# Optimization experiments

Measured on AMD Instinct MI355X. Metric: run time of the kernel, lower is better.

The kernel has to match this reference:

```python
import jax, jax.numpy as jnp
import numpy as np

EMB = 1024
HID = 1024
VOCAB = 32000
SEQ = 128


def _lstm_cell(x, h, c, W_ih, W_hh, b_ih, b_hh):
    # PyTorch gate order: input, forget, cell(g), output
    gates = x @ W_ih.T + b_ih + h @ W_hh.T + b_hh  # [4H]
    i, f, g, o = jnp.split(gates, 4)
    c_new = jax.nn.sigmoid(f) * c + jax.nn.sigmoid(i) * jnp.tanh(g)
    h_new = jax.nn.sigmoid(o) * jnp.tanh(c_new)
    return h_new, c_new


def setup_inputs() -> dict:
    key = jax.random.key(0)
    ks = jax.random.split(key, 12)
    s_emb = 0.02
    s_lstm = 1.0 / np.sqrt(HID)
    return {
        "sentence": jax.random.randint(ks[0], (SEQ,), 0, VOCAB),
        "given_num": 64,
        "emb": jax.random.normal(ks[1], (VOCAB, EMB), jnp.float32) * s_emb,
        "W_ih_lstm": jax.random.normal(ks[2], (4 * HID, EMB), jnp.float32) * s_lstm,
        "W_hh_lstm": jax.random.normal(ks[3], (4 * HID, HID), jnp.float32) * s_lstm,
        "b_ih_lstm": jax.random.normal(ks[4], (4 * HID,), jnp.float32) * s_lstm,
        "b_hh_lstm": jax.random.normal(ks[5], (4 * HID,), jnp.float32) * s_lstm,
        "W_ih_cell": jax.random.normal(ks[6], (4 * HID, EMB), jnp.float32) * s_lstm,
        "W_hh_cell": jax.random.normal(ks[7], (4 * HID, HID), jnp.float32) * s_lstm,
        "b_ih_cell": jax.random.normal(ks[8], (4 * HID,), jnp.float32) * s_lstm,
        "b_hh_cell": jax.random.normal(ks[9], (4 * HID,), jnp.float32) * s_lstm,
        "W_tag": jax.random.normal(ks[10], (VOCAB, HID), jnp.float32) * s_lstm,
        "b_tag": jax.random.normal(ks[11], (VOCAB,), jnp.float32) * s_lstm,
    }


def reference(sentence, given_num, emb, W_ih_lstm, W_hh_lstm, b_ih_lstm, b_hh_lstm,
              W_ih_cell, W_hh_cell, b_ih_cell, b_hh_cell, W_tag, b_tag):
    given_num = int(given_num)  # static (batch-1 rollout, fixed split point)

    # ---- teacher-forced prefix through nn.LSTM (init_hidden -> zeros) ----
    embeds_existing = emb[sentence[:given_num]]  # [g, E]

    def prefix_step(carry, x):
        h, c = carry
        h, c = _lstm_cell(x, h, c, W_ih_lstm, W_hh_lstm, b_ih_lstm, b_hh_lstm)
        return (h, c), h

    h0 = jnp.zeros((HID,), embeds_existing.dtype)
    (h, c), lstm_out = jax.lax.scan(prefix_step, (h0, h0), embeds_existing)
    tag_prefix = lstm_out @ W_tag.T + b_tag  # [g, V]

    # multinomial over softmax(tag) == categorical over logits; only last row's
    # sample is consumed as x_t
    skeys = jax.random.split(jax.random.key(123), SEQ - given_num + 1)
    x_t = jax.random.categorical(skeys[0], tag_prefix[-1])

    def rollout_step(carry, k):
        x_t, h, c = carry
        e = emb[x_t]
        h, c = _lstm_cell(e, h, c, W_ih_cell, W_hh_cell, b_ih_cell, b_hh_cell)
        logits = h @ W_tag.T + b_tag  # [V]
        x_next = jax.random.categorical(k, logits)
        return (x_next, h, c), logits

    _, tag_roll = jax.lax.scan(rollout_step, (x_t, h, c), skeys[1:])  # [S-g, V]

    tag_space = jnp.concatenate([tag_prefix, tag_roll], axis=0)  # [S, V]
    return jax.nn.log_softmax(tag_space, axis=-1)
```

## Files before the change

kernel.cpp:

```cpp
#include <hip/hip_runtime.h>
#include <cstdint>
#include <cstddef>

#define EMBD 1024
#define HIDD 1024
#define G4   4096
#define VOC  32000
#define SEQL 128
#define GN   64
#define NR   64

#define JAX_PARTITIONABLE 1

__device__ __forceinline__ uint32_t rotl32(uint32_t v, int d) { return (v << d) | (v >> (32 - d)); }

__device__ inline void threefry2x32(uint32_t k0, uint32_t k1, uint32_t x0, uint32_t x1,
                                    uint32_t& o0, uint32_t& o1) {
  uint32_t ks2 = k0 ^ k1 ^ 0x1BD11BDAu;
#define TF_ROUND(r) { x0 += x1; x1 = rotl32(x1, r); x1 ^= x0; }
  x0 += k0;  x1 += k1;
  TF_ROUND(13) TF_ROUND(15) TF_ROUND(26) TF_ROUND(6)
  x0 += k1;  x1 += ks2 + 1u;
  TF_ROUND(17) TF_ROUND(29) TF_ROUND(16) TF_ROUND(24)
  x0 += ks2; x1 += k0 + 2u;
  TF_ROUND(13) TF_ROUND(15) TF_ROUND(26) TF_ROUND(6)
  x0 += k0;  x1 += k1 + 3u;
  TF_ROUND(17) TF_ROUND(29) TF_ROUND(16) TF_ROUND(24)
  x0 += k1;  x1 += ks2 + 4u;
  TF_ROUND(13) TF_ROUND(15) TF_ROUND(26) TF_ROUND(6)
  x0 += ks2; x1 += k0 + 5u;
#undef TF_ROUND
  o0 = x0; o1 = x1;
}

__device__ inline uint32_t rng_bits(uint32_t k0, uint32_t k1, uint32_t idx) {
#if JAX_PARTITIONABLE
  uint32_t h0, h1; threefry2x32(k0, k1, 0u, idx, h0, h1);
  return h0 ^ h1;
#else
  uint32_t h0, h1;
  if (idx < (VOC / 2)) { threefry2x32(k0, k1, idx, idx + (VOC / 2), h0, h1); return h0; }
  else                 { threefry2x32(k0, k1, idx - (VOC / 2), idx, h0, h1); return h1; }
#endif
}

__device__ inline float gumbel_of(uint32_t k0, uint32_t k1, uint32_t idx) {
  uint32_t bits = rng_bits(k0, k1, idx);
  float u = __uint_as_float((bits >> 9) | 0x3f800000u) - 1.0f;
  u = fmaxf(u, 1.17549435e-38f);
  return -logf(-logf(u));
}

__device__ inline unsigned long long packCand(float v, int idx) {
  uint32_t u = __float_as_uint(v);
  u = (u & 0x80000000u) ? ~u : (u | 0x80000000u);
  return ((unsigned long long)u << 32) | (unsigned long long)(0xFFFFFFFFu - (uint32_t)idx);
}

__device__ inline float sigf(float x) { return 1.0f / (1.0f + expf(-x)); }

__global__ void k_init(uint2* keys, unsigned* counters, float* cbuf, float* h0) {
  int t = threadIdx.x;
#if JAX_PARTITIONABLE
  if (t < NR + 1) {
    uint32_t a, b; threefry2x32(0u, 123u, 0u, (uint32_t)t, a, b);
    keys[t] = make_uint2(a, b);
  }
#else
  __shared__ uint32_t buf[2 * (NR + 1)];
  if (t < NR + 1) {
    uint32_t a, b; threefry2x32(0u, 123u, (uint32_t)t, (uint32_t)(t + NR + 1), a, b);
    buf[t] = a; buf[t + NR + 1] = b;
  }
  __syncthreads();
  if (t < NR + 1) keys[t] = make_uint2(buf[2 * t], buf[2 * t + 1]);
#endif
  for (int i = t; i < 66; i += 256) counters[i] = 0u;
  for (int i = t; i < HIDD; i += 256) { cbuf[i] = 0.0f; h0[i] = 0.0f; }
}

__global__ void k_gather(const float* __restrict__ emb, const int* __restrict__ sent,
                         float* __restrict__ X) {
  int m = blockIdx.x;
  int row = sent[m];
  const float4* s = (const float4*)(emb + (size_t)row * EMBD);
  float4* d = (float4*)(X + (size_t)m * EMBD);
  d[threadIdx.x] = s[threadIdx.x];
}

__global__ __launch_bounds__(256) void k_gemm64(const float* __restrict__ A,
                                                const float* __restrict__ B,
                                                const float* __restrict__ bias,
                                                float* __restrict__ C, int ldc) {
  __shared__ float As[64][33];
  __shared__ float Bs[64][33];
  int n0 = blockIdx.x * 64;
  int tn = threadIdx.x & 15, tm = threadIdx.x >> 4;
  float acc[4][4] = {{0.f}};
  for (int k0 = 0; k0 < 1024; k0 += 32) {
    for (int f = threadIdx.x; f < 512; f += 256) {
      int r = f >> 3, c4 = (f & 7) << 2;
      float4 v = *(const float4*)(A + (size_t)r * 1024 + k0 + c4);
      As[r][c4 + 0] = v.x; As[r][c4 + 1] = v.y; As[r][c4 + 2] = v.z; As[r][c4 + 3] = v.w;
      float4 u = *(const float4*)(B + (size_t)(n0 + r) * 1024 + k0 + c4);
      Bs[r][c4 + 0] = u.x; Bs[r][c4 + 1] = u.y; Bs[r][c4 + 2] = u.z; Bs[r][c4 + 3] = u.w;
    }
    __syncthreads();
#pragma unroll
    for (int kk = 0; kk < 32; ++kk) {
      float a0 = As[tm * 4 + 0][kk], a1 = As[tm * 4 + 1][kk];
      float a2 = As[tm * 4 + 2][kk], a3 = As[tm * 4 + 3][kk];
      float b0 = Bs[tn * 4 + 0][kk], b1 = Bs[tn * 4 + 1][kk];
      float b2 = Bs[tn * 4 + 2][kk], b3 = Bs[tn * 4 + 3][kk];
      acc[0][0] += a0 * b0; acc[0][1] += a0 * b1; acc[0][2] += a0 * b2; acc[0][3] += a0 * b3;
      acc[1][0] += a1 * b0; acc[1][1] += a1 * b1; acc[1][2] += a1 * b2; acc[1][3] += a1 * b3;
      acc[2][0] += a2 * b0; acc[2][1] += a2 * b1; acc[2][2] += a2 * b2; acc[2][3] += a2 * b3;
      acc[3][0] += a3 * b0; acc[3][1] += a3 * b1; acc[3][2] += a3 * b2; acc[3][3] += a3 * b3;
    }
    __syncthreads();
  }
#pragma unroll
  for (int i = 0; i < 4; ++i)
#pragma unroll
    for (int j = 0; j < 4; ++j) {
      int m = tm * 4 + i, n = n0 + tn * 4 + j;
      float r = acc[i][j] + (bias ? bias[n] : 0.0f);
      C[(size_t)m * ldc + n] = r;
    }
}

__global__ __launch_bounds__(256) void k_lstm_pre(const float* __restrict__ Whh,
                                                  const float* __restrict__ bih,
                                                  const float* __restrict__ bhh,
                                                  const float* __restrict__ gx, int t,
                                                  const float* __restrict__ hprev,
                                                  float* __restrict__ cbuf,
                                                  float* __restrict__ hout) {
  __shared__ float gs[4];
  int wave = threadIdx.x >> 6, lane = threadIdx.x & 63;
  int j = blockIdx.x;
  int r = j + (wave << 10);
  const float4* h4 = (const float4*)hprev;
  const float4* w4 = (const float4*)(Whh + (size_t)r * 1024);
  float a = 0.0f;
#pragma unroll
  for (int q = 0; q < 4; ++q) {
    float4 w = w4[lane + (q << 6)];
    float4 h = h4[lane + (q << 6)];
    a += w.x * h.x + w.y * h.y + w.z * h.z + w.w * h.w;
  }
#pragma unroll
  for (int off = 32; off; off >>= 1) a += __shfl_xor(a, off, 64);
  if (lane == 0) gs[wave] = a + gx[(size_t)t * G4 + r] + bih[r] + bhh[r];
  __syncthreads();
  if (threadIdx.x == 0) {
    float gi = gs[0], gf = gs[1], gg = gs[2], go = gs[3];
    float cn = sigf(gf) * cbuf[j] + sigf(gi) * tanhf(gg);
    cbuf[j] = cn;
    hout[j] = sigf(go) * tanhf(cn);
  }
}

__global__ __launch_bounds__(256) void k_lstm_roll(const float* __restrict__ Wih,
                                                   const float* __restrict__ Whh,
                                                   const float* __restrict__ bih,
                                                   const float* __restrict__ bhh,
                                                   const float* __restrict__ emb,
                                                   const int* __restrict__ tok, int t,
                                                   const float* __restrict__ hprev,
                                                   float* __restrict__ cbuf,
                                                   float* __restrict__ hout) {
  __shared__ float gs[4];
  int wave = threadIdx.x >> 6, lane = threadIdx.x & 63;
  int j = blockIdx.x;
  int r = j + (wave << 10);
  int row = tok[t];
  const float4* x4 = (const float4*)(emb + (size_t)row * EMBD);
  const float4* h4 = (const float4*)hprev;
  const float4* wi = (const float4*)(Wih + (size_t)r * 1024);
  const float4* wh = (const float4*)(Whh + (size_t)r * 1024);
  float a = 0.0f;
#pragma unroll
  for (int q = 0; q < 4; ++q) {
    float4 w = wi[lane + (q << 6)];
    float4 x = x4[lane + (q << 6)];
    a += w.x * x.x + w.y * x.y + w.z * x.z + w.w * x.w;
    w = wh[lane + (q << 6)];
    float4 h = h4[lane + (q << 6)];
    a += w.x * h.x + w.y * h.y + w.z * h.z + w.w * h.w;
  }
#pragma unroll
  for (int off = 32; off; off >>= 1) a += __shfl_xor(a, off, 64);
  if (lane == 0) gs[wave] = a + bih[r] + bhh[r];
  __syncthreads();
  if (threadIdx.x == 0) {
    float gi = gs[0], gf = gs[1], gg = gs[2], go = gs[3];
    float cn = sigf(gf) * cbuf[j] + sigf(gi) * tanhf(gg);
    cbuf[j] = cn;
    hout[j] = sigf(go) * tanhf(cn);
  }
}

__global__ __launch_bounds__(256) void k_logits(const float* __restrict__ Wtag,
                                                const float* __restrict__ btag,
                                                const float* __restrict__ h,
                                                float* __restrict__ outrow,
                                                const uint2* __restrict__ keys, int key_idx,
                                                unsigned long long* __restrict__ partials,
                                                unsigned* __restrict__ counter,
                                                int* __restrict__ token_out) {
  __shared__ float sums[64];
  __shared__ unsigned long long red[256];
  __shared__ int amLast;
  int wave = threadIdx.x >> 6, lane = threadIdx.x & 63;
  int r0 = blockIdx.x * 64;
  const float4* h4 = (const float4*)h;
  float4 hv[4];
#pragma unroll
  for (int q = 0; q < 4; ++q) hv[q] = h4[lane + (q << 6)];
  for (int rr = 0; rr < 16; ++rr) {
    int lr = wave * 16 + rr;
    int r = r0 + lr;
    const float4* w4 = (const float4*)(Wtag + (size_t)r * 1024);
    float a = 0.0f;
#pragma unroll
    for (int q = 0; q < 4; ++q) {
      float4 w = w4[lane + (q << 6)];
      a += w.x * hv[q].x + w.y * hv[q].y + w.z * hv[q].z + w.w * hv[q].w;
    }
#pragma unroll
    for (int off = 32; off; off >>= 1) a += __shfl_xor(a, off, 64);
    if (lane == 0) sums[lr] = a;
  }
  __syncthreads();
  unsigned long long best = 0ull;
  if (threadIdx.x < 64) {
    int r = r0 + threadIdx.x;
    float L = sums[threadIdx.x] + btag[r];
    outrow[r] = L;
    uint2 K = keys[key_idx];
    float y = L + gumbel_of(K.x, K.y, (uint32_t)r);
    best = packCand(y, r);
#pragma unroll
    for (int off = 32; off; off >>= 1) {
      unsigned long long o = __shfl_xor(best, off, 64);
      if (o > best) best = o;
    }
    if (threadIdx.x == 0) partials[blockIdx.x] = best;
  }
  __threadfence();
  __syncthreads();
  if (threadIdx.x == 0) amLast = (atomicAdd(counter, 1u) == gridDim.x - 1) ? 1 : 0;
  __syncthreads();
  if (amLast) {
    __threadfence();
    unsigned long long b = 0ull;
    for (int i = threadIdx.x; i < (int)gridDim.x; i += 256) {
      unsigned long long v = *((volatile unsigned long long*)(partials + i));
      if (v > b) b = v;
    }
    red[threadIdx.x] = b;
    __syncthreads();
    for (int s = 128; s; s >>= 1) {
      if (threadIdx.x < s) {
        if (red[threadIdx.x + s] > red[threadIdx.x]) red[threadIdx.x] = red[threadIdx.x + s];
      }
      __syncthreads();
    }
    if (threadIdx.x == 0)
      token_out[0] = (int)(0xFFFFFFFFu - (uint32_t)(red[0] & 0xFFFFFFFFull));
  }
}

__global__ __launch_bounds__(256) void k_sample_row(const float* __restrict__ row,
                                                    const uint2* __restrict__ keys, int key_idx,
                                                    unsigned long long* __restrict__ partials,
                                                    unsigned* __restrict__ counter,
                                                    int* __restrict__ token_out) {
  __shared__ unsigned long long red[256];
  __shared__ int amLast;
  int v = blockIdx.x * 256 + threadIdx.x;
  unsigned long long best = 0ull;
  if (v < VOC) {
    uint2 K = keys[key_idx];
    float y = row[v] + gumbel_of(K.x, K.y, (uint32_t)v);
    best = packCand(y, v);
  }
  red[threadIdx.x] = best;
  __syncthreads();
  for (int s = 128; s; s >>= 1) {
    if (threadIdx.x < s) {
      if (red[threadIdx.x + s] > red[threadIdx.x]) red[threadIdx.x] = red[threadIdx.x + s];
    }
    __syncthreads();
  }
  if (threadIdx.x == 0) partials[blockIdx.x] = red[0];
  __threadfence();
  __syncthreads();
  if (threadIdx.x == 0) amLast = (atomicAdd(counter, 1u) == gridDim.x - 1) ? 1 : 0;
  __syncthreads();
  if (amLast) {
    __threadfence();
    unsigned long long b = 0ull;
    for (int i = threadIdx.x; i < (int)gridDim.x; i += 256) {
      unsigned long long val = *((volatile unsigned long long*)(partials + i));
      if (val > b) b = val;
    }
    red[threadIdx.x] = b;
    __syncthreads();
    for (int s = 128; s; s >>= 1) {
      if (threadIdx.x < s) {
        if (red[threadIdx.x + s] > red[threadIdx.x]) red[threadIdx.x] = red[threadIdx.x + s];
      }
      __syncthreads();
    }
    if (threadIdx.x == 0)
      token_out[0] = (int)(0xFFFFFFFFu - (uint32_t)(red[0] & 0xFFFFFFFFull));
  }
}

__global__ __launch_bounds__(256) void k_logsoftmax(float* __restrict__ C) {
  __shared__ float red[256];
  float* row = C + (size_t)blockIdx.x * VOC;
  float m = -INFINITY;
  for (int i = threadIdx.x; i < VOC; i += 256) m = fmaxf(m, row[i]);
  red[threadIdx.x] = m;
  __syncthreads();
  for (int s = 128; s; s >>= 1) {
    if (threadIdx.x < s) red[threadIdx.x] = fmaxf(red[threadIdx.x], red[threadIdx.x + s]);
    __syncthreads();
  }
  m = red[0];
  __syncthreads();
  float sum = 0.0f;
  for (int i = threadIdx.x; i < VOC; i += 256) sum += expf(row[i] - m);
  red[threadIdx.x] = sum;
  __syncthreads();
  for (int s = 128; s; s >>= 1) {
    if (threadIdx.x < s) red[threadIdx.x] += red[threadIdx.x + s];
    __syncthreads();
  }
  float lse = m + logf(red[0]);
  __syncthreads();
  for (int i = threadIdx.x; i < VOC; i += 256) row[i] = row[i] - lse;
}

extern "C" void kernel_launch(void* const* d_in, const int* in_sizes, int n_in,
                              void* d_out, int out_size, void* d_ws, size_t ws_size,
                              hipStream_t stream) {
  (void)in_sizes; (void)n_in; (void)out_size; (void)ws_size;
  const int*   sent  = (const int*)  d_in[0];
  const float* emb   = (const float*)d_in[2];
  const float* Wih_l = (const float*)d_in[3];
  const float* Whh_l = (const float*)d_in[4];
  const float* bih_l = (const float*)d_in[5];
  const float* bhh_l = (const float*)d_in[6];
  const float* Wih_c = (const float*)d_in[7];
  const float* Whh_c = (const float*)d_in[8];
  const float* bih_c = (const float*)d_in[9];
  const float* bhh_c = (const float*)d_in[10];
  const float* Wtag  = (const float*)d_in[11];
  const float* btag  = (const float*)d_in[12];
  float* out = (float*)d_out;

  char* ws = (char*)d_ws;
  uint2*              keys     = (uint2*)(ws + 0);
  int*                tokens   = (int*)(ws + 1024);
  unsigned*           counters = (unsigned*)(ws + 2048);
  unsigned long long* partials = (unsigned long long*)(ws + 4096);
  float*              cbuf     = (float*)(ws + 8192);
  float*              h0       = (float*)(ws + 12288);
  float*              lstm_out = (float*)(ws + 16384);
  float*              hroll    = (float*)(ws + 16384 + 262144);
  float*              X        = (float*)(ws + 16384 + 2 * 262144);
  float*              gx       = (float*)(ws + 16384 + 3 * 262144);

  k_init<<<1, 256, 0, stream>>>(keys, counters, cbuf, h0);
  k_gather<<<GN, 256, 0, stream>>>(emb, sent, X);
  k_gemm64<<<G4 / 64, 256, 0, stream>>>(X, Wih_l, nullptr, gx, G4);
  for (int t = 0; t < GN; ++t) {
    const float* hp = t ? (lstm_out + (size_t)(t - 1) * HIDD) : h0;
    k_lstm_pre<<<HIDD, 256, 0, stream>>>(Whh_l, bih_l, bhh_l, gx, t, hp, cbuf,
                                         lstm_out + (size_t)t * HIDD);
  }
  k_gemm64<<<VOC / 64, 256, 0, stream>>>(lstm_out, Wtag, btag, out, VOC);
  k_sample_row<<<(VOC + 255) / 256, 256, 0, stream>>>(out + (size_t)(GN - 1) * VOC, keys, 0,
                                                      partials, counters + 64, tokens);
  for (int t = 0; t < NR; ++t) {
    const float* hp = t ? (hroll + (size_t)(t - 1) * HIDD) : (lstm_out + (size_t)(GN - 1) * HIDD);
    k_lstm_roll<<<HIDD, 256, 0, stream>>>(Wih_c, Whh_c, bih_c, bhh_c, emb, tokens, t, hp, cbuf,
                                          hroll + (size_t)t * HIDD);
    k_logits<<<VOC / 64, 256, 0, stream>>>(Wtag, btag, hroll + (size_t)t * HIDD,
                                           out + (size_t)(GN + t) * VOC, keys, 1 + t,
                                           partials, counters + t, tokens + t + 1);
  }
  k_logsoftmax<<<SEQL, 256, 0, stream>>>(out);
}
```

Before: 5.351 ms.

## Store W_tag as fp16 for logits GEMV and prefix GEMM

Each call converts the vocabulary projection matrix W_tag once to fp16 in workspace. The prefix GEMM and the per-step rollout logits kernel then read the half-size copy and accumulate in fp32. The rollout kernel is rewritten as a wave-per-row GEMV over 32 rows per block, with the partials area enlarged to fit more blocks. The goal is to halve the memory traffic of the bandwidth-bound per-token logits pass. The cost is an extra conversion pass, and the rounded weights may flip sampled tokens relative to the fp32 reference.

```diff
diff --git a/kernel.cpp b/kernel.cpp
--- a/kernel.cpp
+++ b/kernel.cpp
@@ -1,4 +1,5 @@
 #include <hip/hip_runtime.h>
+#include <hip/hip_fp16.h>
 #include <cstdint>
 #include <cstddef>
 
@@ -59,6 +60,11 @@
 
 __device__ inline float sigf(float x) { return 1.0f / (1.0f + expf(-x)); }
 
+__device__ __forceinline__ float h2f(unsigned short u) {
+  __half_raw hr; hr.x = u;
+  return __half2float(__half(hr));
+}
+
 __global__ void k_init(uint2* keys, unsigned* counters, float* cbuf, float* h0) {
   int t = threadIdx.x;
 #if JAX_PARTITIONABLE
@@ -77,6 +83,26 @@
 #endif
   for (int i = t; i < 66; i += 256) counters[i] = 0u;
   for (int i = t; i < HIDD; i += 256) { cbuf[i] = 0.0f; h0[i] = 0.0f; }
+}
+
+__global__ __launch_bounds__(256) void k_cvt_f16(const float* __restrict__ src,
+                                                 unsigned short* __restrict__ dst, int n) {
+  int stride = gridDim.x * blockDim.x * 8;
+  for (int i = (blockIdx.x * blockDim.x + threadIdx.x) * 8; i < n; i += stride) {
+    float4 a = *(const float4*)(src + i);
+    float4 b = *(const float4*)(src + i + 4);
+    union { unsigned short u[8]; uint4 v; } p;
+    __half t;
+    t = __float2half(a.x); p.u[0] = __half_raw(t).x;
+    t = __float2half(a.y); p.u[1] = __half_raw(t).x;
+    t = __float2half(a.z); p.u[2] = __half_raw(t).x;
+    t = __float2half(a.w); p.u[3] = __half_raw(t).x;
+    t = __float2half(b.x); p.u[4] = __half_raw(t).x;
+    t = __float2half(b.y); p.u[5] = __half_raw(t).x;
+    t = __float2half(b.z); p.u[6] = __half_raw(t).x;
+    t = __float2half(b.w); p.u[7] = __half_raw(t).x;
+    *(uint4*)(dst + i) = p.v;
+  }
 }
 
 __global__ void k_gather(const float* __restrict__ emb, const int* __restrict__ sent,
@@ -104,6 +130,53 @@
       As[r][c4 + 0] = v.x; As[r][c4 + 1] = v.y; As[r][c4 + 2] = v.z; As[r][c4 + 3] = v.w;
       float4 u = *(const float4*)(B + (size_t)(n0 + r) * 1024 + k0 + c4);
       Bs[r][c4 + 0] = u.x; Bs[r][c4 + 1] = u.y; Bs[r][c4 + 2] = u.z; Bs[r][c4 + 3] = u.w;
+    }
+    __syncthreads();
+#pragma unroll
+    for (int kk = 0; kk < 32; ++kk) {
+      float a0 = As[tm * 4 + 0][kk], a1 = As[tm * 4 + 1][kk];
+      float a2 = As[tm * 4 + 2][kk], a3 = As[tm * 4 + 3][kk];
+      float b0 = Bs[tn * 4 + 0][kk], b1 = Bs[tn * 4 + 1][kk];
+      float b2 = Bs[tn * 4 + 2][kk], b3 = Bs[tn * 4 + 3][kk];
+      acc[0][0] += a0 * b0; acc[0][1] += a0 * b1; acc[0][2] += a0 * b2; acc[0][3] += a0 * b3;
+      acc[1][0] += a1 * b0; acc[1][1] += a1 * b1; acc[1][2] += a1 * b2; acc[1][3] += a1 * b3;
+      acc[2][0] += a2 * b0; acc[2][1] += a2 * b1; acc[2][2] += a2 * b2; acc[2][3] += a2 * b3;
+      acc[3][0] += a3 * b0; acc[3][1] += a3 * b1; acc[3][2] += a3 * b2; acc[3][3] += a3 * b3;
+    }
+    __syncthreads();
+  }
+#pragma unroll
+  for (int i = 0; i < 4; ++i)
+#pragma unroll
+    for (int j = 0; j < 4; ++j) {
+      int m = tm * 4 + i, n = n0 + tn * 4 + j;
+      float r = acc[i][j] + (bias ? bias[n] : 0.0f);
+      C[(size_t)m * ldc + n] = r;
+    }
+}
+
+__global__ __launch_bounds__(256) void k_gemm64_f16b(const float* __restrict__ A,
+                                                     const unsigned short* __restrict__ B16,
+                                                     const float* __restrict__ bias,
+                                                     float* __restrict__ C, int ldc) {
+  __shared__ float As[64][33];
+  __shared__ float Bs[64][33];
+  int n0 = blockIdx.x * 64;
+  int tn = threadIdx.x & 15, tm = threadIdx.x >> 4;
+  float acc[4][4] = {{0.f}};
+  for (int k0 = 0; k0 < 1024; k0 += 32) {
+    for (int f = threadIdx.x; f < 512; f += 256) {
+      int r = f >> 3, c4 = (f & 7) << 2;
+      float4 v = *(const float4*)(A + (size_t)r * 1024 + k0 + c4);
+      As[r][c4 + 0] = v.x; As[r][c4 + 1] = v.y; As[r][c4 + 2] = v.z; As[r][c4 + 3] = v.w;
+    }
+    {
+      int f = threadIdx.x;
+      int r = f >> 2, c8 = (f & 3) << 3;
+      union { uint4 v; unsigned short u[8]; } p;
+      p.v = *(const uint4*)(B16 + (size_t)(n0 + r) * 1024 + k0 + c8);
+#pragma unroll
+      for (int j = 0; j < 8; ++j) Bs[r][c8 + j] = h2f(p.u[j]);
     }
     __syncthreads();
 #pragma unroll
@@ -272,6 +345,87 @@
   }
 }
 
+__global__ __launch_bounds__(256) void k_logits_f16(const unsigned short* __restrict__ Wt16,
+                                                    const float* __restrict__ btag,
+                                                    const float* __restrict__ h,
+                                                    float* __restrict__ outrow,
+                                                    const uint2* __restrict__ keys, int key_idx,
+                                                    unsigned long long* __restrict__ partials,
+                                                    unsigned* __restrict__ counter,
+                                                    int* __restrict__ token_out) {
+  __shared__ float sums[32];
+  __shared__ unsigned long long red[256];
+  __shared__ int amLast;
+  int wave = threadIdx.x >> 6, lane = threadIdx.x & 63;
+  int r0 = blockIdx.x * 32;
+  const float4* h4 = (const float4*)h;
+  float4 hq[4];
+#pragma unroll
+  for (int q = 0; q < 2; ++q) {
+    hq[2 * q]     = h4[q * 128 + lane * 2];
+    hq[2 * q + 1] = h4[q * 128 + lane * 2 + 1];
+  }
+  for (int rr = 0; rr < 8; ++rr) {
+    int lr = wave * 8 + rr;
+    int r = r0 + lr;
+    const unsigned short* wrow = Wt16 + (size_t)r * 1024;
+    float a = 0.0f;
+#pragma unroll
+    for (int q = 0; q < 2; ++q) {
+      union { uint4 v; unsigned short u[8]; } p;
+      p.v = *(const uint4*)(wrow + q * 512 + lane * 8);
+      float4 hA = hq[2 * q], hB = hq[2 * q + 1];
+      a += h2f(p.u[0]) * hA.x; a += h2f(p.u[1]) * hA.y;
+      a += h2f(p.u[2]) * hA.z; a += h2f(p.u[3]) * hA.w;
+      a += h2f(p.u[4]) * hB.x; a += h2f(p.u[5]) * hB.y;
+      a += h2f(p.u[6]) * hB.z; a += h2f(p.u[7]) * hB.w;
+    }
+#pragma unroll
+    for (int off = 32; off; off >>= 1) a += __shfl_xor(a, off, 64);
+    if (lane == 0) sums[lr] = a;
+  }
+  __syncthreads();
+  unsigned long long best = 0ull;
+  if (threadIdx.x < 64) {
+    if (threadIdx.x < 32) {
+      int r = r0 + threadIdx.x;
+      float L = sums[threadIdx.x] + btag[r];
+      outrow[r] = L;
+      uint2 K = keys[key_idx];
+      float y = L + gumbel_of(K.x, K.y, (uint32_t)r);
+      best = packCand(y, r);
+    }
+#pragma unroll
+    for (int off = 32; off; off >>= 1) {
+      unsigned long long o = __shfl_xor(best, off, 64);
+      if (o > best) best = o;
+    }
+    if (threadIdx.x == 0) partials[blockIdx.x] = best;
+  }
+  __threadfence();
+  __syncthreads();
+  if (threadIdx.x == 0) amLast = (atomicAdd(counter, 1u) == gridDim.x - 1) ? 1 : 0;
+  __syncthreads();
+  if (amLast) {
+    __threadfence();
+    unsigned long long b = 0ull;
+    for (int i = threadIdx.x; i < (int)gridDim.x; i += 256) {
+      unsigned long long v = *((volatile unsigned long long*)(partials + i));
+      if (v > b) b = v;
+    }
+    red[threadIdx.x] = b;
+    __syncthreads();
+    for (int s = 128; s; s >>= 1) {
+      if (threadIdx.x < s) {
+        if (red[threadIdx.x + s] > red[threadIdx.x]) red[threadIdx.x] = red[threadIdx.x + s];
+      }
+      __syncthreads();
+    }
+    if (threadIdx.x == 0)
+      token_out[0] = (int)(0xFFFFFFFFu - (uint32_t)(red[0] & 0xFFFFFFFFull));
+  }
+}
+
 __global__ __launch_bounds__(256) void k_sample_row(const float* __restrict__ row,
                                                     const uint2* __restrict__ keys, int key_idx,
                                                     unsigned long long* __restrict__ partials,
@@ -348,7 +502,7 @@
 extern "C" void kernel_launch(void* const* d_in, const int* in_sizes, int n_in,
                               void* d_out, int out_size, void* d_ws, size_t ws_size,
                               hipStream_t stream) {
-  (void)in_sizes; (void)n_in; (void)out_size; (void)ws_size;
+  (void)in_sizes; (void)n_in; (void)out_size;
   const int*   sent  = (const int*)  d_in[0];
   const float* emb   = (const float*)d_in[2];
   const float* Wih_l = (const float*)d_in[3];
@@ -368,14 +522,20 @@
   int*                tokens   = (int*)(ws + 1024);
   unsigned*           counters = (unsigned*)(ws + 2048);
   unsigned long long* partials = (unsigned long long*)(ws + 4096);
-  float*              cbuf     = (float*)(ws + 8192);
-  float*              h0       = (float*)(ws + 12288);
-  float*              lstm_out = (float*)(ws + 16384);
-  float*              hroll    = (float*)(ws + 16384 + 262144);
-  float*              X        = (float*)(ws + 16384 + 2 * 262144);
-  float*              gx       = (float*)(ws + 16384 + 3 * 262144);
+  float*              cbuf     = (float*)(ws + 12288);
+  float*              h0       = (float*)(ws + 16384);
+  float*              lstm_out = (float*)(ws + 20480);
+  float*              hroll    = (float*)(ws + 20480 + 262144);
+  float*              X        = (float*)(ws + 20480 + 2 * 262144);
+  float*              gx       = (float*)(ws + 20480 + 3 * 262144);
+  const size_t WT16_OFF   = 2u * 1024u * 1024u;
+  const size_t WT16_BYTES = (size_t)VOC * 1024u * 2u;
+  unsigned short* Wt16 = (unsigned short*)(ws + WT16_OFF);
+  bool use16 = (ws_size >= WT16_OFF + WT16_BYTES);
 
   k_init<<<1, 256, 0, stream>>>(keys, counters, cbuf, h0);
+  if (use16)
+    k_cvt_f16<<<2048, 256, 0, stream>>>(Wtag, Wt16, VOC * 1024);
   k_gather<<<GN, 256, 0, stream>>>(emb, sent, X);
   k_gemm64<<<G4 / 64, 256, 0, stream>>>(X, Wih_l, nullptr, gx, G4);
   for (int t = 0; t < GN; ++t) {
@@ -383,16 +543,24 @@
     k_lstm_pre<<<HIDD, 256, 0, stream>>>(Whh_l, bih_l, bhh_l, gx, t, hp, cbuf,
                                          lstm_out + (size_t)t * HIDD);
   }
-  k_gemm64<<<VOC / 64, 256, 0, stream>>>(lstm_out, Wtag, btag, out, VOC);
+  if (use16)
+    k_gemm64_f16b<<<VOC / 64, 256, 0, stream>>>(lstm_out, Wt16, btag, out, VOC);
+  else
+    k_gemm64<<<VOC / 64, 256, 0, stream>>>(lstm_out, Wtag, btag, out, VOC);
   k_sample_row<<<(VOC + 255) / 256, 256, 0, stream>>>(out + (size_t)(GN - 1) * VOC, keys, 0,
                                                       partials, counters + 64, tokens);
   for (int t = 0; t < NR; ++t) {
     const float* hp = t ? (hroll + (size_t)(t - 1) * HIDD) : (lstm_out + (size_t)(GN - 1) * HIDD);
     k_lstm_roll<<<HIDD, 256, 0, stream>>>(Wih_c, Whh_c, bih_c, bhh_c, emb, tokens, t, hp, cbuf,
                                           hroll + (size_t)t * HIDD);
-    k_logits<<<VOC / 64, 256, 0, stream>>>(Wtag, btag, hroll + (size_t)t * HIDD,
-                                           out + (size_t)(GN + t) * VOC, keys, 1 + t,
-                                           partials, counters + t, tokens + t + 1);
+    if (use16)
+      k_logits_f16<<<VOC / 32, 256, 0, stream>>>(Wt16, btag, hroll + (size_t)t * HIDD,
+                                                 out + (size_t)(GN + t) * VOC, keys, 1 + t,
+                                                 partials, counters + t, tokens + t + 1);
+    else
+      k_logits<<<VOC / 64, 256, 0, stream>>>(Wtag, btag, hroll + (size_t)t * HIDD,
+                                             out + (size_t)(GN + t) * VOC, keys, 1 + t,
+                                             partials, counters + t, tokens + t + 1);
   }
   k_logsoftmax<<<SEQL, 256, 0, stream>>>(out);
 }
```

Measured after the change: 6.835 ms. 1.28x slower.
